# Kernel optimization log

Hardware: AMD Instinct MI355X
Metric: run time of the kernel (lower is better)

The kernel has to match this reference:

```python
import jax, jax.numpy as jnp
import numpy as np

B, C, H, W = 2, 128, 128, 128
K, STRIDE, DIL, NH = 8, 2, 2, 8
HID = int(C * 4 / 3)  # 170


def _ln(x, g, b):
    # layernorm2d: normalize over channel axis (last axis in NHWC)
    mu = jnp.mean(x, axis=-1, keepdims=True)
    xc = x - mu
    var = jnp.mean(xc * xc, axis=-1, keepdims=True)
    return xc * jax.lax.rsqrt(var + 1e-6) * g + b


def _nat_attn(xn, qkv_w, qkv_b, qg, qb, kg, kb, proj_w, proj_b):
    # dilated/strided local-neighborhood attention (NATTEN-style)
    Bq, Hq, Wq, Cq = xn.shape
    dh = Cq // NH
    qkv = xn @ qkv_w.T + qkv_b
    q, k, v = jnp.split(qkv, 3, axis=-1)
    q = _ln(q, qg, qb)
    k = _ln(k, kg, kb)
    # keys/values on a stride-subsampled grid
    kc = k[:, ::STRIDE, ::STRIDE, :]
    vc = v[:, ::STRIDE, ::STRIDE, :]
    Hc, Wc = Hq // STRIDE, Wq // STRIDE
    plo = DIL * (K // 2)
    phi = DIL * (K - 1 - K // 2)
    pad = ((0, 0), (plo, phi), (plo, phi), (0, 0))
    kp = jnp.pad(kc, pad)
    vp = jnp.pad(vc, pad)
    mp = jnp.pad(jnp.ones((1, Hc, Wc, 1), dtype=bool), pad)
    offs = [(i * DIL, j * DIL) for i in range(K) for j in range(K)]  # fixed k*k window taps
    kn = jnp.stack([kp[:, a:a + Hc, b:b + Wc, :] for a, b in offs], axis=3).reshape(Bq, Hc, Wc, K * K, NH, dh)
    vn = jnp.stack([vp[:, a:a + Hc, b:b + Wc, :] for a, b in offs], axis=3).reshape(Bq, Hc, Wc, K * K, NH, dh)
    mn = jnp.stack([mp[:, a:a + Hc, b:b + Wc, 0] for a, b in offs], axis=3)  # [1,Hc,Wc,kk]
    # each full-res query maps to its coarse kv cell: [B,Hc,stride,Wc,stride,heads,dh]
    q6 = q.reshape(Bq, Hc, STRIDE, Wc, STRIDE, NH, dh)
    scores = jnp.einsum('bisjtnd,bijknd->bisjtnk', q6, kn) * (dh ** -0.5)
    m = mn[:, :, None, :, None, None, :]
    scores = jnp.where(m, scores, jnp.float32(-1e30))
    attn = jax.nn.softmax(scores, axis=-1)
    out = jnp.einsum('bisjtnk,bijknd->bisjtnd', attn, vn).reshape(Bq, Hq, Wq, Cq)
    return out @ proj_w.T + proj_b


def _cffn(xn, fc1_w, fc1_b, mg, mb, fc2_w, fc2_b):
    h = xn @ fc1_w.T + fc1_b
    h = _ln(h, mg, mb)
    h = jax.nn.gelu(h, approximate=True)  # gelu_tanh
    return h @ fc2_w.T + fc2_b


def setup_inputs():
    key = jax.random.key(0)
    ks = jax.random.split(key, 6)
    w = lambda k, shp: jax.random.normal(k, shp, dtype=jnp.float32) * 0.02
    z = lambda n: jnp.zeros((n,), jnp.float32)
    o = lambda n: jnp.ones((n,), jnp.float32)
    return {
        'x': jax.random.normal(ks[0], (B, C, H, W), dtype=jnp.float32),
        'qkv_w': w(ks[1], (3 * C, C)), 'qkv_b': z(3 * C),
        'qg': o(C), 'qb': z(C), 'kg': o(C), 'kb': z(C),
        'proj_w': w(ks[2], (C, C)), 'proj_b': z(C),
        'n1g': o(C), 'n1b': z(C), 'n2g': o(C), 'n2b': z(C),
        'ls1_g': jnp.full((C,), 1e-5, jnp.float32),
        'ls2_g': jnp.full((C,), 1e-5, jnp.float32),
        'fc1_w': w(ks[3], (HID, C)), 'fc1_b': z(HID),
        'mg': o(HID), 'mb': z(HID),
        'fc2_w': w(ks[4], (C, HID)), 'fc2_b': z(C),
    }


def reference(x, qkv_w, qkv_b, qg, qb, kg, kb, proj_w, proj_b, n1g, n1b, n2g, n2b, ls1_g, ls2_g, fc1_w, fc1_b, mg, mb, fc2_w, fc2_b):
    xh = jnp.transpose(x, (0, 2, 3, 1))  # NCHW -> NHWC
    xh = xh + ls1_g * _nat_attn(_ln(xh, n1g, n1b), qkv_w, qkv_b, qg, qb, kg, kb, proj_w, proj_b)
    xh = xh + ls2_g * _cffn(_ln(xh, n2g, n2b), fc1_w, fc1_b, mg, mb, fc2_w, fc2_b)
    return jnp.transpose(xh, (0, 3, 1, 2))
```

## Files before the change

kernel.cpp:

```cpp
#include <hip/hip_runtime.h>
#include <hip/hip_bf16.h>

typedef __hip_bfloat16 BF;
typedef __attribute__((ext_vector_type(8))) short bf16x8;
typedef __attribute__((ext_vector_type(4))) float f32x4;
typedef __attribute__((ext_vector_type(4))) unsigned short us4;


#define ASTR 200
#define KSTR 136

__device__ __forceinline__ short bfr(float f){
  union{float f; unsigned u;} c; c.f = f;
  const unsigned u = c.u + 0x7FFFu + ((c.u >> 16) & 1u);
  return (short)(u >> 16);
}
__device__ __forceinline__ bf16x8 pk8(float4 a, float4 b){
  bf16x8 r;
  r[0]=bfr(a.x); r[1]=bfr(a.y); r[2]=bfr(a.z); r[3]=bfr(a.w);
  r[4]=bfr(b.x); r[5]=bfr(b.y); r[6]=bfr(b.z); r[7]=bfr(b.w);
  return r;
}

__device__ __forceinline__ void gsum16h(float v[16], float* red, int tid){
  #pragma unroll
  for(int s = 1; s < 64; s <<= 1){
    #pragma unroll
    for(int i = 0; i < 16; i++) v[i] += __shfl_xor(v[i], s);
  }
  const int wid = tid >> 6, half = tid >> 7;
  __syncthreads();
  if((tid & 63) == 0){
    #pragma unroll
    for(int i = 0; i < 16; i++) red[wid*16 + i] = v[i];
  }
  __syncthreads();
  #pragma unroll
  for(int i = 0; i < 16; i++) v[i] = red[half*32 + i] + red[half*32 + 16 + i];
}

__device__ __forceinline__ void rowredh(float s1[4], float s2[4], float* red, int tid){
  const int lane = tid & 63, wid = tid >> 6, half = tid >> 7;
  #pragma unroll
  for(int m = 1; m < 16; m <<= 1){
    #pragma unroll
    for(int r = 0; r < 4; r++){ s1[r] += __shfl_xor(s1[r], m); s2[r] += __shfl_xor(s2[r], m); }
  }
  const int q4 = lane >> 4;
  __syncthreads();
  if((lane & 15) == 0){
    #pragma unroll
    for(int r = 0; r < 4; r++){
      red[wid*32 + q4*4 + r]      = s1[r];
      red[wid*32 + 16 + q4*4 + r] = s2[r];
    }
  }
  __syncthreads();
  #pragma unroll
  for(int r = 0; r < 4; r++){
    s1[r] = red[half*64 + q4*4 + r]      + red[half*64 + 32 + q4*4 + r];
    s2[r] = red[half*64 + 16 + q4*4 + r] + red[half*64 + 48 + q4*4 + r];
  }
}

__device__ __forceinline__ void rowred4(float s1[4], float s2[4], float* red,
                                        int wave, int lane){
  #pragma unroll
  for(int m = 1; m < 16; m <<= 1){
    #pragma unroll
    for(int r = 0; r < 4; r++){ s1[r] += __shfl_xor(s1[r], m); s2[r] += __shfl_xor(s2[r], m); }
  }
  const int q4 = lane >> 4;
  __syncthreads();
  if((lane & 15) == 0){
    #pragma unroll
    for(int r = 0; r < 4; r++){
      red[wave*32 + q4*4 + r]      = s1[r];
      red[wave*32 + 16 + q4*4 + r] = s2[r];
    }
  }
  __syncthreads();
  #pragma unroll
  for(int r = 0; r < 4; r++){
    s1[r] = red[q4*4 + r] + red[32 + q4*4 + r] + red[64 + q4*4 + r] + red[96 + q4*4 + r];
    s2[r] = red[16 + q4*4 + r] + red[48 + q4*4 + r] + red[80 + q4*4 + r] + red[112 + q4*4 + r];
  }
}

__global__ void __launch_bounds__(256)
k_pre(const float* __restrict__ x,
      const float* __restrict__ qkv_w, const float* __restrict__ proj_w,
      const float* __restrict__ fc1_w, const float* __restrict__ fc2_w,
      const float* __restrict__ qkv_b,
      const float* __restrict__ kg, const float* __restrict__ kb,
      const float* __restrict__ n1g, const float* __restrict__ n1b,
      float* __restrict__ xt, BF* __restrict__ pk,
      float* __restrict__ kcb, float* __restrict__ vcb){
  __shared__ __align__(16) unsigned char sm[16640];
  const int bx = blockIdx.x, tid = threadIdx.x;

  if(bx >= 952){
    float (*tile)[65] = (float(*)[65])sm;
    const int bxt = bx - 952;
    const int b = bxt >> 9, r2 = bxt & 511;
    const int pb = (r2 & 255) * 64, cb = (r2 >> 8) * 64;
    const int tx = tid & 63, ty = tid >> 6;
    #pragma unroll
    for(int r = 0; r < 64; r += 4)
      tile[ty+r][tx] = x[(size_t)(b*128 + cb+ty+r)*16384 + pb + tx];
    __syncthreads();
    #pragma unroll
    for(int r = 0; r < 64; r += 4)
      xt[(size_t)((b<<14) + pb + ty + r)*128 + cb + tx] = tile[tx][ty+r];
    return;
  }
  if(bx >= 512){
    const int idx = (bx - 512) * 256 + tid;
    if(idx >= 112640) return;
    float val;
    if(idx < 49152){
      const int reg = idx >> 14, l = idx & 16383;
      const int j = l & 7, q = (l>>3)&3, n = (l>>5)&127, s = l>>12;
      val = qkv_w[(reg*128 + n)*128 + (s*32 + q*8 + j)];
    } else if(idx < 65536){
      const int l = idx - 49152;
      const int j = l&7, q=(l>>3)&3, n=(l>>5)&127, s=l>>12;
      val = proj_w[n*128 + (s*32+q*8+j)];
    } else if(idx < 88064){
      const int l = idx - 65536;
      const int j = l&7, q=(l>>3)&3, rem = l>>5;
      const int n = rem % 176, s = rem / 176;
      const int k = s*32+q*8+j;
      val = (n < 170) ? fc1_w[n*128 + k] : 0.f;
    } else {
      const int l = idx - 88064;
      const int j = l&7, q=(l>>3)&3, n=(l>>5)&127, s=l>>12;
      const int k = s*32+q*8+j;
      val = (k < 170) ? fc2_w[n*170 + k] : 0.f;
    }
    pk[idx] = __float2bfloat16(val);
    return;
  }

  BF* const Abuf = (BF*)sm;
  float* const red = (float*)(sm + 8704);
  const int lane = tid & 63, half = tid >> 7, wh = (tid >> 6) & 1, c = tid & 127;
  const int l15 = lane & 15, q4 = lane >> 4;
  const int cp0 = bx * 16;
  const int b = cp0 >> 12, ic = (cp0 & 4095) >> 6, jb = cp0 & 63;
  BF* const AbufH = Abuf + half*16*KSTR;

  float xv[8];
  {
    const size_t off = (size_t)(b*128 + c)*16384 + (size_t)(2*ic)*128 + 2*(jb + half*8);
    const float4* xp4 = (const float4*)(x + off);
    const float4 f0 = xp4[0], f1 = xp4[1], f2 = xp4[2], f3 = xp4[3];
    xv[0]=f0.x; xv[1]=f0.z; xv[2]=f1.x; xv[3]=f1.z;
    xv[4]=f2.x; xv[5]=f2.z; xv[6]=f3.x; xv[7]=f3.z;
  }
  float st[16];
  #pragma unroll
  for(int r = 0; r < 8; r++){ st[r] = xv[r]; st[8+r] = xv[r]*xv[r]; }
  gsum16h(st, red, tid);
  {
    const float g = n1g[c], be = n1b[c];
    #pragma unroll
    for(int r = 0; r < 8; r++){
      const float mu = st[r]*(1.f/128.f);
      const float var = st[8+r]*(1.f/128.f) - mu*mu;
      AbufH[r*KSTR + c] = __float2bfloat16((xv[r]-mu)*rsqrtf(var+1e-6f)*g + be);
    }
  }
  __syncthreads();
  bf16x8 af[4];
  #pragma unroll
  for(int s = 0; s < 4; s++) af[s] = *(const bf16x8*)&AbufH[l15*KSTR + s*32 + q4*8];

  f32x4 acc[4];
  #pragma unroll
  for(int nt = 0; nt < 4; nt++){ acc[nt][0]=0.f; acc[nt][1]=0.f; acc[nt][2]=0.f; acc[nt][3]=0.f; }
  #pragma unroll
  for(int nt = 0; nt < 4; nt++){
    const int n = (wh*4+nt)*16 + l15;
    #pragma unroll
    for(int s = 0; s < 4; s++){
      const float* wp = qkv_w + (size_t)(128 + n)*128 + s*32 + q4*8;
      acc[nt] = __builtin_amdgcn_mfma_f32_16x16x32_bf16(
        af[s], pk8(*(const float4*)wp, *(const float4*)(wp+4)), acc[nt], 0,0,0);
    }
  }
  float s1[4], s2[4];
  #pragma unroll
  for(int r = 0; r < 4; r++){ s1[r]=0.f; s2[r]=0.f; }
  #pragma unroll
  for(int nt = 0; nt < 4; nt++){
    const float colb = qkv_b[128 + (wh*4+nt)*16 + l15];
    #pragma unroll
    for(int r = 0; r < 4; r++){
      const float vv = acc[nt][r] + colb;
      acc[nt][r] = vv; s1[r] += vv; s2[r] += vv*vv;
    }
  }
  rowredh(s1, s2, red, tid);
  #pragma unroll
  for(int nt = 0; nt < 4; nt++){
    const int col = (wh*4+nt)*16 + l15;
    const float g = kg[col], be = kb[col];
    #pragma unroll
    for(int r = 0; r < 4; r++){
      const int row = q4*4 + r;
      if(row < 8){
        const float mu = s1[r]*(1.f/128.f);
        const float var = s2[r]*(1.f/128.f) - mu*mu;
        kcb[(size_t)(cp0 + half*8 + row)*128 + col] = (acc[nt][r]-mu)*rsqrtf(var+1e-6f)*g + be;
      }
    }
  }
  #pragma unroll
  for(int nt = 0; nt < 4; nt++){ acc[nt][0]=0.f; acc[nt][1]=0.f; acc[nt][2]=0.f; acc[nt][3]=0.f; }
  #pragma unroll
  for(int nt = 0; nt < 4; nt++){
    const int n = (wh*4+nt)*16 + l15;
    #pragma unroll
    for(int s = 0; s < 4; s++){
      const float* wp = qkv_w + (size_t)(256 + n)*128 + s*32 + q4*8;
      acc[nt] = __builtin_amdgcn_mfma_f32_16x16x32_bf16(
        af[s], pk8(*(const float4*)wp, *(const float4*)(wp+4)), acc[nt], 0,0,0);
    }
  }
  #pragma unroll
  for(int nt = 0; nt < 4; nt++){
    const int col = (wh*4+nt)*16 + l15;
    const float bv = qkv_b[256 + col];
    #pragma unroll
    for(int r = 0; r < 4; r++){
      const int row = q4*4 + r;
      if(row < 8) vcb[(size_t)(cp0 + half*8 + row)*128 + col] = acc[nt][r] + bv;
    }
  }
}

__global__ void __launch_bounds__(256, 5)
k_cell(const float* __restrict__ xt_in,
       const BF* __restrict__ packQ, const BF* __restrict__ packP,
       const BF* __restrict__ packF1, const BF* __restrict__ packF2,
       const float* __restrict__ qkv_b,
       const float* __restrict__ qg, const float* __restrict__ qb,
       const float* __restrict__ n1g, const float* __restrict__ n1b,
       const float* __restrict__ proj_b,
       const float* __restrict__ ls1, const float* __restrict__ ls2,
       const float* __restrict__ n2g, const float* __restrict__ n2b,
       const float* __restrict__ fc1_b,
       const float* __restrict__ mg, const float* __restrict__ mb,
       const float* __restrict__ fc2_b,
       const float* __restrict__ kcb, const float* __restrict__ vcb,
       float* __restrict__ out){
  __shared__ __align__(16) BF uni[9216];
  BF* const Abuf = uni;
  __shared__ float xvL[2048];
  __shared__ __align__(16) ushort qnH[2176];
  __shared__ ushort cidx2[256];
  float* const red = (float*)qnH;
  const int tid = threadIdx.x, wave = tid>>6, lane = tid&63;
  const int l15 = lane & 15, q4 = lane >> 4;

  const int bx0 = blockIdx.x;
  const int bx = ((bx0 & 7) << 8) | (bx0 >> 3);
  const int b = bx >> 10, rem = bx & 1023, ip = rem >> 5, jq = rem & 31;
  const size_t p0 = (size_t)b*2097152 + (size_t)(512*ip + 4*jq)*128;
  const int c = tid & 127, half = tid >> 7;

  float xv[8];
  #pragma unroll
  for(int r = 0; r < 8; r++){
    const int p = half*8 + r;
    const size_t pr = p0 + ((size_t)(p>>2)<<14) + (size_t)((p&3)<<7);
    xv[r] = xt_in[pr + c];
    xvL[p*128 + c] = xv[r];
  }
  {
    const int cell = tid >> 6, e = tid & 63;
    const int i = e >> 3, j = e & 7;
    const int ic = 2*ip + (cell>>1), jcc = 2*jq + (cell&1);
    const int ri = ic + 2*i - 8, rj = jcc + 2*j - 8;
    const bool ok = (rj >= 0) && (rj < 64) && (ri >= 0) && (ri < 64);
    cidx2[cell*64 + e] = ok ? (ushort)(b*4096 + ri*64 + rj) : (ushort)0;
  }

  float st[16];
  #pragma unroll
  for(int r = 0; r < 8; r++){ st[r] = xv[r]; st[8+r] = xv[r]*xv[r]; }
  gsum16h(st, red, tid);
  {
    const float g = n1g[c], be = n1b[c];
    #pragma unroll
    for(int r = 0; r < 8; r++){
      const int p = half*8 + r;
      const float mu = st[r]*(1.f/128.f);
      const float var = st[8+r]*(1.f/128.f) - mu*mu;
      Abuf[p*ASTR + c] = __float2bfloat16((xv[r]-mu)*rsqrtf(var+1e-6f)*g + be);
    }
  }
  __syncthreads();

  {
    bf16x8 af[4];
    #pragma unroll
    for(int s = 0; s < 4; s++) af[s] = *(const bf16x8*)&Abuf[l15*ASTR + s*32 + q4*8];
    f32x4 acc[2];
    #pragma unroll
    for(int nt = 0; nt < 2; nt++){ acc[nt][0]=0.f; acc[nt][1]=0.f; acc[nt][2]=0.f; acc[nt][3]=0.f; }
    #pragma unroll
    for(int nt = 0; nt < 2; nt++){
      const int n = (wave*2+nt)*16 + l15;
      #pragma unroll
      for(int s = 0; s < 4; s++){
        bf16x8 bf = *(const bf16x8*)&packQ[((s*128 + n)*4 + q4)*8];
        acc[nt] = __builtin_amdgcn_mfma_f32_16x16x32_bf16(af[s], bf, acc[nt], 0,0,0);
      }
    }
    float s1[4], s2[4];
    #pragma unroll
    for(int r = 0; r < 4; r++){ s1[r]=0.f; s2[r]=0.f; }
    #pragma unroll
    for(int nt = 0; nt < 2; nt++){
      const float cb2 = qkv_b[(wave*2+nt)*16 + l15];
      #pragma unroll
      for(int r = 0; r < 4; r++){
        const float vv = acc[nt][r] + cb2;
        acc[nt][r] = vv; s1[r] += vv; s2[r] += vv*vv;
      }
    }
    rowred4(s1, s2, red, wave, lane);
    short tw[2][4];
    {
      float mu[4], rs[4];
      #pragma unroll
      for(int r = 0; r < 4; r++){
        mu[r] = s1[r]*(1.f/128.f);
        rs[r] = rsqrtf(s2[r]*(1.f/128.f) - mu[r]*mu[r] + 1e-6f);
      }
      #pragma unroll
      for(int nt = 0; nt < 2; nt++){
        const int col = (wave*2+nt)*16 + l15;
        const float g = qg[col], be = qb[col];
        #pragma unroll
        for(int r = 0; r < 4; r++)
          tw[nt][r] = bfr((acc[nt][r]-mu[r])*rs[r]*g + be);
      }
    }
    __syncthreads();
    #pragma unroll
    for(int nt = 0; nt < 2; nt++){
      const int col = (wave*2+nt)*16 + l15;
      const int colp = col + (col >> 4);
      #pragma unroll
      for(int r = 0; r < 4; r++){
        const int cell = 2*(q4>>1) + ((r>>1)&1);
        const int lp   = 2*(q4&1) + (r&1);
        qnH[cell*544 + colp*4 + lp] = (ushort)tw[nt][r];
      }
    }
  }
  __syncthreads();

  const int hsub = l15 >> 2, px = l15 & 3;
  const int par = q4 >> 1, dbase = (q4 & 1) * 8;
  BF* const attw = uni + wave*2304;
  ushort* const Vt = (ushort*)attw;
  ushort* const Pb = (ushort*)(attw + 1152);
  const ushort* cidx = cidx2 + wave*64;
  const ushort* qp = qnH + wave*544;
  const int ic = 2*ip + (wave>>1), jcc = 2*jq + (wave&1);
  const int i0 = l15 >> 3;
  const int rj = jcc + 2*(l15 & 7) - 8;
  const bool vj = (rj >= 0) && (rj < 64);
  float madd[4];
  #pragma unroll
  for(int nt = 0; nt < 4; nt++){
    const int ri = ic + 2*(nt*2 + i0) - 8;
    madd[nt] = (vj && ri >= 0 && ri < 64) ? 0.f : -1e30f;
  }

  f32x4 oC[2];
  #pragma unroll
  for(int hg = 0; hg < 2; hg++){
    bf16x8 afq0, afq1;
    {
      const int idx0 = (hg*64 + hsub*16 + dbase + (hg*4 + hsub))*4 + px;
      short bq[8];
      #pragma unroll
      for(int j = 0; j < 8; j++) bq[j] = (short)qp[idx0 + 4*j];
      const bool a0 = (par == hsub), a1 = ((2 + par) == hsub);
      #pragma unroll
      for(int j = 0; j < 8; j++){
        afq0[j] = a0 ? bq[j] : (short)0;
        afq1[j] = a1 ? bq[j] : (short)0;
      }
    }
    f32x4 accq[4];
    #pragma unroll
    for(int nt = 0; nt < 4; nt++){ accq[nt][0]=0.f; accq[nt][1]=0.f; accq[nt][2]=0.f; accq[nt][3]=0.f; }
    #pragma unroll
    for(int nt = 0; nt < 4; nt++){
      const float* kp = kcb + ((size_t)cidx[nt*16 + l15] << 7) + hg*64 + q4*8;
      const float4 k00 = *(const float4*)kp;
      const float4 k01 = *(const float4*)(kp + 4);
      const float4 k10 = *(const float4*)(kp + 32);
      const float4 k11 = *(const float4*)(kp + 36);
      accq[nt] = __builtin_amdgcn_mfma_f32_16x16x32_bf16(afq0, pk8(k00,k01), accq[nt], 0,0,0);
      accq[nt] = __builtin_amdgcn_mfma_f32_16x16x32_bf16(afq1, pk8(k10,k11), accq[nt], 0,0,0);
    }
    float inv[4];
    #pragma unroll
    for(int reg = 0; reg < 4; reg++){
      const float s0 = accq[0][reg]*0.25f + madd[0];
      const float s1 = accq[1][reg]*0.25f + madd[1];
      const float s2 = accq[2][reg]*0.25f + madd[2];
      const float s3 = accq[3][reg]*0.25f + madd[3];
      float m = fmaxf(fmaxf(s0,s1), fmaxf(s2,s3));
      #pragma unroll
      for(int sft = 1; sft < 16; sft <<= 1) m = fmaxf(m, __shfl_xor(m, sft));
      const float e0 = __expf(s0-m), e1 = __expf(s1-m);
      const float e2 = __expf(s2-m), e3 = __expf(s3-m);
      ushort* pr = Pb + (q4*4 + reg)*72 + l15;
      pr[0]  = (ushort)bfr(e0);
      pr[16] = (ushort)bfr(e1);
      pr[32] = (ushort)bfr(e2);
      pr[48] = (ushort)bfr(e3);
      float es = e0+e1+e2+e3;
      #pragma unroll
      for(int sft = 1; sft < 16; sft <<= 1) es += __shfl_xor(es, sft);
      inv[reg] = 1.f/es;
    }
    const bf16x8 pa0 = *(const bf16x8*)(Pb + l15*72 + q4*8);
    const bf16x8 pa1 = *(const bf16x8*)(Pb + l15*72 + 32 + q4*8);

    f32x4 oSel; oSel[0]=0.f; oSel[1]=0.f; oSel[2]=0.f; oSel[3]=0.f;
    #pragma unroll
    for(int hs = 0; hs < 4; hs++){
      const int h = hg*4 + hs;
      float4 vv[4];
      #pragma unroll
      for(int it = 0; it < 4; it++)
        vv[it] = *(const float4*)(vcb + ((size_t)cidx[l15*4 + it] << 7) + h*16 + q4*4);
      #pragma unroll
      for(int dd = 0; dd < 4; dd++){
        us4 w;
        w[0] = (unsigned short)bfr(((const float*)&vv[0])[dd]);
        w[1] = (unsigned short)bfr(((const float*)&vv[1])[dd]);
        w[2] = (unsigned short)bfr(((const float*)&vv[2])[dd]);
        w[3] = (unsigned short)bfr(((const float*)&vv[3])[dd]);
        *(us4*)(Vt + (q4*4 + dd)*72 + l15*4) = w;
      }
      const bf16x8 bv0 = *(const bf16x8*)(Vt + l15*72 + q4*8);
      const bf16x8 bv1 = *(const bf16x8*)(Vt + l15*72 + 32 + q4*8);
      f32x4 accv; accv[0]=0.f; accv[1]=0.f; accv[2]=0.f; accv[3]=0.f;
      accv = __builtin_amdgcn_mfma_f32_16x16x32_bf16(pa0, bv0, accv, 0,0,0);
      accv = __builtin_amdgcn_mfma_f32_16x16x32_bf16(pa1, bv1, accv, 0,0,0);
      if(q4 == hs){ oSel[0]=accv[0]; oSel[1]=accv[1]; oSel[2]=accv[2]; oSel[3]=accv[3]; }
    }
    oC[hg][0] = oSel[0]*inv[0]; oC[hg][1] = oSel[1]*inv[1];
    oC[hg][2] = oSel[2]*inv[2]; oC[hg][3] = oSel[3]*inv[3];
  }
  __syncthreads();
  {
    ushort* ab = (ushort*)Abuf;
    #pragma unroll
    for(int hg = 0; hg < 2; hg++){
      const int col = (hg*4 + q4)*16 + l15;
      #pragma unroll
      for(int reg = 0; reg < 4; reg++){
        const int row_p = 8*(wave>>1) + 4*(reg>>1) + 2*(wave&1) + (reg&1);
        ab[row_p*ASTR + col] = (ushort)bfr(oC[hg][reg]);
      }
    }
  }
  __syncthreads();

  float xh[2][4];
  {
    bf16x8 af[4];
    #pragma unroll
    for(int s = 0; s < 4; s++) af[s] = *(const bf16x8*)&Abuf[l15*ASTR + s*32 + q4*8];
    f32x4 acc[2];
    #pragma unroll
    for(int nt = 0; nt < 2; nt++){ acc[nt][0]=0.f; acc[nt][1]=0.f; acc[nt][2]=0.f; acc[nt][3]=0.f; }
    #pragma unroll
    for(int nt = 0; nt < 2; nt++){
      const int n = (wave*2+nt)*16 + l15;
      #pragma unroll
      for(int s = 0; s < 4; s++){
        bf16x8 bf = *(const bf16x8*)&packP[((s*128 + n)*4 + q4)*8];
        acc[nt] = __builtin_amdgcn_mfma_f32_16x16x32_bf16(af[s], bf, acc[nt], 0,0,0);
      }
    }
    float s1[4], s2[4];
    #pragma unroll
    for(int r = 0; r < 4; r++){ s1[r]=0.f; s2[r]=0.f; }
    #pragma unroll
    for(int nt = 0; nt < 2; nt++){
      const int col = (wave*2+nt)*16 + l15;
      const float bp = proj_b[col], l1 = ls1[col];
      #pragma unroll
      for(int r = 0; r < 4; r++){
        const int p = q4*4 + r;
        const float hx = xvL[p*128 + col] + l1*(acc[nt][r] + bp);
        xh[nt][r] = hx; s1[r] += hx; s2[r] += hx*hx;
      }
    }
    rowred4(s1, s2, red, wave, lane);
    #pragma unroll
    for(int nt = 0; nt < 2; nt++){
      const int col = (wave*2+nt)*16 + l15;
      const float g2 = n2g[col], be = n2b[col];
      #pragma unroll
      for(int r = 0; r < 4; r++){
        const int p = q4*4 + r;
        const float mu = s1[r]*(1.f/128.f);
        const float var = s2[r]*(1.f/128.f) - mu*mu;
        Abuf[p*ASTR + col] =
          __float2bfloat16((xh[nt][r]-mu)*rsqrtf(var+1e-6f)*g2 + be);
      }
    }
  }
  __syncthreads();

  {
    bf16x8 af[4];
    #pragma unroll
    for(int s = 0; s < 4; s++) af[s] = *(const bf16x8*)&Abuf[l15*ASTR + s*32 + q4*8];
    const int NT1 = (wave < 3) ? 3 : 2;
    const int tb  = (wave < 3) ? wave*3 : 9;
    f32x4 acc1[3];
    #pragma unroll
    for(int nt = 0; nt < 3; nt++){ acc1[nt][0]=0.f; acc1[nt][1]=0.f; acc1[nt][2]=0.f; acc1[nt][3]=0.f; }
    for(int nt = 0; nt < NT1; nt++){
      const int n = (tb + nt)*16 + l15;
      #pragma unroll
      for(int s = 0; s < 4; s++){
        bf16x8 bf = *(const bf16x8*)&packF1[((s*176 + n)*4 + q4)*8];
        acc1[nt] = __builtin_amdgcn_mfma_f32_16x16x32_bf16(af[s], bf, acc1[nt], 0,0,0);
      }
    }
    float s1[4], s2[4];
    #pragma unroll
    for(int r = 0; r < 4; r++){ s1[r]=0.f; s2[r]=0.f; }
    for(int nt = 0; nt < NT1; nt++){
      const int col = (tb + nt)*16 + l15;
      const float b1 = (col < 170) ? fc1_b[col] : 0.f;
      #pragma unroll
      for(int r = 0; r < 4; r++){
        const float vv = acc1[nt][r] + b1;
        acc1[nt][r] = vv; s1[r] += vv; s2[r] += vv*vv;
      }
    }
    rowred4(s1, s2, red, wave, lane);
    for(int z = tid; z < 352; z += 256){
      const int row = z / 22, colz = 170 + (z - (z/22)*22);
      Abuf[row*ASTR + colz] = __float2bfloat16(0.f);
    }
    const float kA = 0.7978845608028654f, kB = 0.044715f;
    for(int nt = 0; nt < NT1; nt++){
      const int col = (tb + nt)*16 + l15;
      if(col < 170){
        const float g2 = mg[col], be = mb[col];
        #pragma unroll
        for(int r = 0; r < 4; r++){
          const int p = q4*4 + r;
          const float mu = s1[r]*(1.f/170.f);
          const float var = s2[r]*(1.f/170.f) - mu*mu;
          const float hn = (acc1[nt][r]-mu)*rsqrtf(var+1e-6f)*g2 + be;
          const float u = kA*(hn + kB*hn*hn*hn);
          const float gl = hn / (1.f + __expf(-2.f*u));
          Abuf[p*ASTR + col] = __float2bfloat16(gl);
        }
      }
    }
  }
  __syncthreads();

  {
    bf16x8 af[6];
    #pragma unroll
    for(int s = 0; s < 6; s++) af[s] = *(const bf16x8*)&Abuf[l15*ASTR + s*32 + q4*8];
    f32x4 acc[2];
    #pragma unroll
    for(int nt = 0; nt < 2; nt++){ acc[nt][0]=0.f; acc[nt][1]=0.f; acc[nt][2]=0.f; acc[nt][3]=0.f; }
    #pragma unroll
    for(int nt = 0; nt < 2; nt++){
      const int n = (wave*2+nt)*16 + l15;
      #pragma unroll
      for(int s = 0; s < 6; s++){
        bf16x8 bf = *(const bf16x8*)&packF2[((s*128 + n)*4 + q4)*8];
        acc[nt] = __builtin_amdgcn_mfma_f32_16x16x32_bf16(af[s], bf, acc[nt], 0,0,0);
      }
    }
    #pragma unroll
    for(int nt = 0; nt < 2; nt++){
      const int col = (wave*2+nt)*16 + l15;
      const float bf2 = fc2_b[col], l2 = ls2[col];
      float4 o4;
      o4.x = xh[nt][0] + l2*(acc[nt][0] + bf2);
      o4.y = xh[nt][1] + l2*(acc[nt][1] + bf2);
      o4.z = xh[nt][2] + l2*(acc[nt][2] + bf2);
      o4.w = xh[nt][3] + l2*(acc[nt][3] + bf2);
      *(float4*)(out + (size_t)(b*128 + col)*16384 + (size_t)(4*ip + q4)*128 + 4*jq) = o4;
    }
  }
}

extern "C" void kernel_launch(void* const* d_in, const int* in_sizes, int n_in,
                              void* d_out, int out_size, void* d_ws, size_t ws_size,
                              hipStream_t stream){
  const float* x      = (const float*)d_in[0];
  const float* qkv_w  = (const float*)d_in[1];
  const float* qkv_b  = (const float*)d_in[2];
  const float* qg     = (const float*)d_in[3];
  const float* qb     = (const float*)d_in[4];
  const float* kg     = (const float*)d_in[5];
  const float* kb     = (const float*)d_in[6];
  const float* proj_w = (const float*)d_in[7];
  const float* proj_b = (const float*)d_in[8];
  const float* n1g    = (const float*)d_in[9];
  const float* n1b    = (const float*)d_in[10];
  const float* n2g    = (const float*)d_in[11];
  const float* n2b    = (const float*)d_in[12];
  const float* ls1    = (const float*)d_in[13];
  const float* ls2    = (const float*)d_in[14];
  const float* fc1_w  = (const float*)d_in[15];
  const float* fc1_b  = (const float*)d_in[16];
  const float* mg     = (const float*)d_in[17];
  const float* mb     = (const float*)d_in[18];
  const float* fc2_w  = (const float*)d_in[19];
  const float* fc2_b  = (const float*)d_in[20];

  float* ws  = (float*)d_ws;
  float* xt  = ws;
  float* kcb = ws + 4194304;
  float* vcb = ws + 5242880;
  BF* pk     = (BF*)(ws + 6291456);
  BF* packQ  = pk;
  BF* packP  = pk + 49152;
  BF* packF1 = pk + 65536;
  BF* packF2 = pk + 88064;

  k_pre <<<1976, 256, 0, stream>>>(x, qkv_w, proj_w, fc1_w, fc2_w, qkv_b,
                                   kg, kb, n1g, n1b, xt, pk, kcb, vcb);
  k_cell<<<2048, 256, 0, stream>>>(xt, packQ, packP, packF1, packF2,
                                   qkv_b, qg, qb, n1g, n1b, proj_b, ls1, ls2,
                                   n2g, n2b, fc1_b, mg, mb, fc2_b,
                                   kcb, vcb, (float*)d_out);
}
```

Measured before the change: 234.4 us.

## Fuse pre and cell kernels into one persistent cooperative kernel with grid sync

Merges the preprocessing kernel (K/V projection, transpose, weight packing) and the per-cell attention/FFN kernel into a single cooperative launch of 1280 blocks. The blocks finish the pre-work, hit a grid-wide barrier, then loop over the 2048 cell units. The pre-work is redistributed so some blocks handle two transpose tiles, and a two-kernel path is kept in case the cooperative launch fails. This removes one kernel launch and its tail gap, at the cost of a grid barrier, the restrictions of cooperative launch, and possible load imbalance because units do not divide evenly across blocks.

```diff
diff --git a/kernel.cpp b/kernel.cpp
--- a/kernel.cpp
+++ b/kernel.cpp
@@ -1,5 +1,8 @@
 #include <hip/hip_runtime.h>
+#include <hip/hip_cooperative_groups.h>
 #include <hip/hip_bf16.h>
+
+namespace cg = cooperative_groups;
 
 typedef __hip_bfloat16 BF;
 typedef __attribute__((ext_vector_type(8))) short bf16x8;
@@ -9,6 +12,14 @@
 
 #define ASTR 200
 #define KSTR 136
+
+struct KP {
+  const float *x, *qkv_w, *proj_w, *fc1_w, *fc2_w, *qkv_b;
+  const float *qg, *qb, *kg, *kb, *n1g, *n1b, *proj_b, *ls1, *ls2;
+  const float *n2g, *n2b, *fc1_b, *mg, *mb, *fc2_b;
+  float *xt, *kcb, *vcb, *out;
+  BF *pk;
+};
 
 __device__ __forceinline__ short bfr(float f){
   union{float f; unsigned u;} c; c.f = f;
@@ -87,185 +98,168 @@
   }
 }
 
-__global__ void __launch_bounds__(256)
-k_pre(const float* __restrict__ x,
-      const float* __restrict__ qkv_w, const float* __restrict__ proj_w,
-      const float* __restrict__ fc1_w, const float* __restrict__ fc2_w,
-      const float* __restrict__ qkv_b,
-      const float* __restrict__ kg, const float* __restrict__ kb,
-      const float* __restrict__ n1g, const float* __restrict__ n1b,
-      float* __restrict__ xt, BF* __restrict__ pk,
-      float* __restrict__ kcb, float* __restrict__ vcb){
-  __shared__ __align__(16) unsigned char sm[16640];
-  const int bx = blockIdx.x, tid = threadIdx.x;
-
-  if(bx >= 952){
-    float (*tile)[65] = (float(*)[65])sm;
-    const int bxt = bx - 952;
-    const int b = bxt >> 9, r2 = bxt & 511;
+__device__ __forceinline__ void pre_work(const KP& P, BF* uni, float* red){
+  const int bid = blockIdx.x, tid = threadIdx.x;
+  if(bid < 512){
+    BF* const Abuf = uni;
+    const int lane = tid & 63, half = tid >> 7, wh = (tid >> 6) & 1, c = tid & 127;
+    const int l15 = lane & 15, q4 = lane >> 4;
+    const int cp0 = bid * 16;
+    const int b = cp0 >> 12, ic = (cp0 & 4095) >> 6, jb = cp0 & 63;
+    BF* const AbufH = Abuf + half*16*KSTR;
+
+    float xv[8];
+    {
+      const size_t off = (size_t)(b*128 + c)*16384 + (size_t)(2*ic)*128 + 2*(jb + half*8);
+      const float4* xp4 = (const float4*)(P.x + off);
+      const float4 f0 = xp4[0], f1 = xp4[1], f2 = xp4[2], f3 = xp4[3];
+      xv[0]=f0.x; xv[1]=f0.z; xv[2]=f1.x; xv[3]=f1.z;
+      xv[4]=f2.x; xv[5]=f2.z; xv[6]=f3.x; xv[7]=f3.z;
+    }
+    float st[16];
+    #pragma unroll
+    for(int r = 0; r < 8; r++){ st[r] = xv[r]; st[8+r] = xv[r]*xv[r]; }
+    gsum16h(st, red, tid);
+    {
+      const float g = P.n1g[c], be = P.n1b[c];
+      #pragma unroll
+      for(int r = 0; r < 8; r++){
+        const float mu = st[r]*(1.f/128.f);
+        const float var = st[8+r]*(1.f/128.f) - mu*mu;
+        AbufH[r*KSTR + c] = __float2bfloat16((xv[r]-mu)*rsqrtf(var+1e-6f)*g + be);
+      }
+    }
+    __syncthreads();
+    bf16x8 af[4];
+    #pragma unroll
+    for(int s = 0; s < 4; s++) af[s] = *(const bf16x8*)&AbufH[l15*KSTR + s*32 + q4*8];
+
+    f32x4 acc[4];
+    #pragma unroll
+    for(int nt = 0; nt < 4; nt++){ acc[nt][0]=0.f; acc[nt][1]=0.f; acc[nt][2]=0.f; acc[nt][3]=0.f; }
+    #pragma unroll
+    for(int nt = 0; nt < 4; nt++){
+      const int n = (wh*4+nt)*16 + l15;
+      #pragma unroll
+      for(int s = 0; s < 4; s++){
+        const float* wp = P.qkv_w + (size_t)(128 + n)*128 + s*32 + q4*8;
+        acc[nt] = __builtin_amdgcn_mfma_f32_16x16x32_bf16(
+          af[s], pk8(*(const float4*)wp, *(const float4*)(wp+4)), acc[nt], 0,0,0);
+      }
+    }
+    float s1[4], s2[4];
+    #pragma unroll
+    for(int r = 0; r < 4; r++){ s1[r]=0.f; s2[r]=0.f; }
+    #pragma unroll
+    for(int nt = 0; nt < 4; nt++){
+      const float colb = P.qkv_b[128 + (wh*4+nt)*16 + l15];
+      #pragma unroll
+      for(int r = 0; r < 4; r++){
+        const float vv = acc[nt][r] + colb;
+        acc[nt][r] = vv; s1[r] += vv; s2[r] += vv*vv;
+      }
+    }
+    rowredh(s1, s2, red, tid);
+    #pragma unroll
+    for(int nt = 0; nt < 4; nt++){
+      const int col = (wh*4+nt)*16 + l15;
+      const float g = P.kg[col], be = P.kb[col];
+      #pragma unroll
+      for(int r = 0; r < 4; r++){
+        const int row = q4*4 + r;
+        if(row < 8){
+          const float mu = s1[r]*(1.f/128.f);
+          const float var = s2[r]*(1.f/128.f) - mu*mu;
+          P.kcb[(size_t)(cp0 + half*8 + row)*128 + col] =
+            (acc[nt][r]-mu)*rsqrtf(var+1e-6f)*g + be;
+        }
+      }
+    }
+    #pragma unroll
+    for(int nt = 0; nt < 4; nt++){ acc[nt][0]=0.f; acc[nt][1]=0.f; acc[nt][2]=0.f; acc[nt][3]=0.f; }
+    #pragma unroll
+    for(int nt = 0; nt < 4; nt++){
+      const int n = (wh*4+nt)*16 + l15;
+      #pragma unroll
+      for(int s = 0; s < 4; s++){
+        const float* wp = P.qkv_w + (size_t)(256 + n)*128 + s*32 + q4*8;
+        acc[nt] = __builtin_amdgcn_mfma_f32_16x16x32_bf16(
+          af[s], pk8(*(const float4*)wp, *(const float4*)(wp+4)), acc[nt], 0,0,0);
+      }
+    }
+    #pragma unroll
+    for(int nt = 0; nt < 4; nt++){
+      const int col = (wh*4+nt)*16 + l15;
+      const float bv = P.qkv_b[256 + col];
+      #pragma unroll
+      for(int r = 0; r < 4; r++){
+        const int row = q4*4 + r;
+        if(row < 8) P.vcb[(size_t)(cp0 + half*8 + row)*128 + col] = acc[nt][r] + bv;
+      }
+    }
+    return;
+  }
+
+  float (*tile)[65] = (float(*)[65])uni;
+  const int t0 = bid - 512;
+  const int ntile = (bid < 768) ? 2 : 1;
+  for(int it = 0; it < ntile; it++){
+    const int t = t0 + it*768;
+    const int b = t >> 9, r2 = t & 511;
     const int pb = (r2 & 255) * 64, cb = (r2 >> 8) * 64;
     const int tx = tid & 63, ty = tid >> 6;
+    if(it) __syncthreads();
     #pragma unroll
     for(int r = 0; r < 64; r += 4)
-      tile[ty+r][tx] = x[(size_t)(b*128 + cb+ty+r)*16384 + pb + tx];
+      tile[ty+r][tx] = P.x[(size_t)(b*128 + cb+ty+r)*16384 + pb + tx];
     __syncthreads();
     #pragma unroll
     for(int r = 0; r < 64; r += 4)
-      xt[(size_t)((b<<14) + pb + ty + r)*128 + cb + tx] = tile[tx][ty+r];
-    return;
-  }
-  if(bx >= 512){
-    const int idx = (bx - 512) * 256 + tid;
-    if(idx >= 112640) return;
-    float val;
-    if(idx < 49152){
-      const int reg = idx >> 14, l = idx & 16383;
-      const int j = l & 7, q = (l>>3)&3, n = (l>>5)&127, s = l>>12;
-      val = qkv_w[(reg*128 + n)*128 + (s*32 + q*8 + j)];
-    } else if(idx < 65536){
-      const int l = idx - 49152;
-      const int j = l&7, q=(l>>3)&3, n=(l>>5)&127, s=l>>12;
-      val = proj_w[n*128 + (s*32+q*8+j)];
-    } else if(idx < 88064){
-      const int l = idx - 65536;
-      const int j = l&7, q=(l>>3)&3, rem = l>>5;
-      const int n = rem % 176, s = rem / 176;
-      const int k = s*32+q*8+j;
-      val = (n < 170) ? fc1_w[n*128 + k] : 0.f;
-    } else {
-      const int l = idx - 88064;
-      const int j = l&7, q=(l>>3)&3, n=(l>>5)&127, s=l>>12;
-      const int k = s*32+q*8+j;
-      val = (k < 170) ? fc2_w[n*170 + k] : 0.f;
-    }
-    pk[idx] = __float2bfloat16(val);
-    return;
-  }
-
-  BF* const Abuf = (BF*)sm;
-  float* const red = (float*)(sm + 8704);
-  const int lane = tid & 63, half = tid >> 7, wh = (tid >> 6) & 1, c = tid & 127;
-  const int l15 = lane & 15, q4 = lane >> 4;
-  const int cp0 = bx * 16;
-  const int b = cp0 >> 12, ic = (cp0 & 4095) >> 6, jb = cp0 & 63;
-  BF* const AbufH = Abuf + half*16*KSTR;
-
-  float xv[8];
-  {
-    const size_t off = (size_t)(b*128 + c)*16384 + (size_t)(2*ic)*128 + 2*(jb + half*8);
-    const float4* xp4 = (const float4*)(x + off);
-    const float4 f0 = xp4[0], f1 = xp4[1], f2 = xp4[2], f3 = xp4[3];
-    xv[0]=f0.x; xv[1]=f0.z; xv[2]=f1.x; xv[3]=f1.z;
-    xv[4]=f2.x; xv[5]=f2.z; xv[6]=f3.x; xv[7]=f3.z;
-  }
-  float st[16];
-  #pragma unroll
-  for(int r = 0; r < 8; r++){ st[r] = xv[r]; st[8+r] = xv[r]*xv[r]; }
-  gsum16h(st, red, tid);
-  {
-    const float g = n1g[c], be = n1b[c];
-    #pragma unroll
-    for(int r = 0; r < 8; r++){
-      const float mu = st[r]*(1.f/128.f);
-      const float var = st[8+r]*(1.f/128.f) - mu*mu;
-      AbufH[r*KSTR + c] = __float2bfloat16((xv[r]-mu)*rsqrtf(var+1e-6f)*g + be);
-    }
-  }
-  __syncthreads();
-  bf16x8 af[4];
-  #pragma unroll
-  for(int s = 0; s < 4; s++) af[s] = *(const bf16x8*)&AbufH[l15*KSTR + s*32 + q4*8];
-
-  f32x4 acc[4];
-  #pragma unroll
-  for(int nt = 0; nt < 4; nt++){ acc[nt][0]=0.f; acc[nt][1]=0.f; acc[nt][2]=0.f; acc[nt][3]=0.f; }
-  #pragma unroll
-  for(int nt = 0; nt < 4; nt++){
-    const int n = (wh*4+nt)*16 + l15;
-    #pragma unroll
-    for(int s = 0; s < 4; s++){
-      const float* wp = qkv_w + (size_t)(128 + n)*128 + s*32 + q4*8;
-      acc[nt] = __builtin_amdgcn_mfma_f32_16x16x32_bf16(
-        af[s], pk8(*(const float4*)wp, *(const float4*)(wp+4)), acc[nt], 0,0,0);
-    }
-  }
-  float s1[4], s2[4];
-  #pragma unroll
-  for(int r = 0; r < 4; r++){ s1[r]=0.f; s2[r]=0.f; }
-  #pragma unroll
-  for(int nt = 0; nt < 4; nt++){
-    const float colb = qkv_b[128 + (wh*4+nt)*16 + l15];
-    #pragma unroll
-    for(int r = 0; r < 4; r++){
-      const float vv = acc[nt][r] + colb;
-      acc[nt][r] = vv; s1[r] += vv; s2[r] += vv*vv;
-    }
-  }
-  rowredh(s1, s2, red, tid);
-  #pragma unroll
-  for(int nt = 0; nt < 4; nt++){
-    const int col = (wh*4+nt)*16 + l15;
-    const float g = kg[col], be = kb[col];
-    #pragma unroll
-    for(int r = 0; r < 4; r++){
-      const int row = q4*4 + r;
-      if(row < 8){
-        const float mu = s1[r]*(1.f/128.f);
-        const float var = s2[r]*(1.f/128.f) - mu*mu;
-        kcb[(size_t)(cp0 + half*8 + row)*128 + col] = (acc[nt][r]-mu)*rsqrtf(var+1e-6f)*g + be;
-      }
-    }
-  }
-  #pragma unroll
-  for(int nt = 0; nt < 4; nt++){ acc[nt][0]=0.f; acc[nt][1]=0.f; acc[nt][2]=0.f; acc[nt][3]=0.f; }
-  #pragma unroll
-  for(int nt = 0; nt < 4; nt++){
-    const int n = (wh*4+nt)*16 + l15;
-    #pragma unroll
-    for(int s = 0; s < 4; s++){
-      const float* wp = qkv_w + (size_t)(256 + n)*128 + s*32 + q4*8;
-      acc[nt] = __builtin_amdgcn_mfma_f32_16x16x32_bf16(
-        af[s], pk8(*(const float4*)wp, *(const float4*)(wp+4)), acc[nt], 0,0,0);
-    }
-  }
-  #pragma unroll
-  for(int nt = 0; nt < 4; nt++){
-    const int col = (wh*4+nt)*16 + l15;
-    const float bv = qkv_b[256 + col];
-    #pragma unroll
-    for(int r = 0; r < 4; r++){
-      const int row = q4*4 + r;
-      if(row < 8) vcb[(size_t)(cp0 + half*8 + row)*128 + col] = acc[nt][r] + bv;
-    }
-  }
-}
-
-__global__ void __launch_bounds__(256, 5)
-k_cell(const float* __restrict__ xt_in,
-       const BF* __restrict__ packQ, const BF* __restrict__ packP,
-       const BF* __restrict__ packF1, const BF* __restrict__ packF2,
-       const float* __restrict__ qkv_b,
-       const float* __restrict__ qg, const float* __restrict__ qb,
-       const float* __restrict__ n1g, const float* __restrict__ n1b,
-       const float* __restrict__ proj_b,
-       const float* __restrict__ ls1, const float* __restrict__ ls2,
-       const float* __restrict__ n2g, const float* __restrict__ n2b,
-       const float* __restrict__ fc1_b,
-       const float* __restrict__ mg, const float* __restrict__ mb,
-       const float* __restrict__ fc2_b,
-       const float* __restrict__ kcb, const float* __restrict__ vcb,
-       float* __restrict__ out){
-  __shared__ __align__(16) BF uni[9216];
-  BF* const Abuf = uni;
-  __shared__ float xvL[2048];
-  __shared__ __align__(16) ushort qnH[2176];
-  __shared__ ushort cidx2[256];
-  float* const red = (float*)qnH;
+      P.xt[(size_t)((b<<14) + pb + ty + r)*128 + cb + tx] = tile[tx][ty+r];
+  }
+  if(bid >= 768){
+    const int idx = (bid - 768) * 256 + tid;
+    if(idx < 112640){
+      float val;
+      if(idx < 49152){
+        const int reg = idx >> 14, l = idx & 16383;
+        const int j = l & 7, q = (l>>3)&3, n = (l>>5)&127, s = l>>12;
+        val = P.qkv_w[(reg*128 + n)*128 + (s*32 + q*8 + j)];
+      } else if(idx < 65536){
+        const int l = idx - 49152;
+        const int j = l&7, q=(l>>3)&3, n=(l>>5)&127, s=l>>12;
+        val = P.proj_w[n*128 + (s*32+q*8+j)];
+      } else if(idx < 88064){
+        const int l = idx - 65536;
+        const int j = l&7, q=(l>>3)&3, rem = l>>5;
+        const int n = rem % 176, s = rem / 176;
+        const int k = s*32+q*8+j;
+        val = (n < 170) ? P.fc1_w[n*128 + k] : 0.f;
+      } else {
+        const int l = idx - 88064;
+        const int j = l&7, q=(l>>3)&3, n=(l>>5)&127, s=l>>12;
+        const int k = s*32+q*8+j;
+        val = (k < 170) ? P.fc2_w[n*170 + k] : 0.f;
+      }
+      P.pk[idx] = __float2bfloat16(val);
+    }
+  }
+}
+
+__device__ __forceinline__ void cell_unit(const KP& P, int u,
+                                          BF* uni, float* xvL,
+                                          ushort* qnH, ushort* cidx2){
   const int tid = threadIdx.x, wave = tid>>6, lane = tid&63;
   const int l15 = lane & 15, q4 = lane >> 4;
-
-  const int bx0 = blockIdx.x;
-  const int bx = ((bx0 & 7) << 8) | (bx0 >> 3);
+  BF* const Abuf = uni;
+  float* const red = (float*)qnH;
+  const BF* packQ  = P.pk;
+  const BF* packP  = P.pk + 49152;
+  const BF* packF1 = P.pk + 65536;
+  const BF* packF2 = P.pk + 88064;
+  __syncthreads();
+
+  const int bx = ((u & 7) << 8) | (u >> 3);
   const int b = bx >> 10, rem = bx & 1023, ip = rem >> 5, jq = rem & 31;
   const size_t p0 = (size_t)b*2097152 + (size_t)(512*ip + 4*jq)*128;
   const int c = tid & 127, half = tid >> 7;
@@ -275,7 +269,7 @@
   for(int r = 0; r < 8; r++){
     const int p = half*8 + r;
     const size_t pr = p0 + ((size_t)(p>>2)<<14) + (size_t)((p&3)<<7);
-    xv[r] = xt_in[pr + c];
+    xv[r] = P.xt[pr + c];
     xvL[p*128 + c] = xv[r];
   }
   {
@@ -292,7 +286,7 @@
   for(int r = 0; r < 8; r++){ st[r] = xv[r]; st[8+r] = xv[r]*xv[r]; }
   gsum16h(st, red, tid);
   {
-    const float g = n1g[c], be = n1b[c];
+    const float g = P.n1g[c], be = P.n1b[c];
     #pragma unroll
     for(int r = 0; r < 8; r++){
       const int p = half*8 + r;
@@ -324,7 +318,7 @@
     for(int r = 0; r < 4; r++){ s1[r]=0.f; s2[r]=0.f; }
     #pragma unroll
     for(int nt = 0; nt < 2; nt++){
-      const float cb2 = qkv_b[(wave*2+nt)*16 + l15];
+      const float cb2 = P.qkv_b[(wave*2+nt)*16 + l15];
       #pragma unroll
       for(int r = 0; r < 4; r++){
         const float vv = acc[nt][r] + cb2;
@@ -343,7 +337,7 @@
       #pragma unroll
       for(int nt = 0; nt < 2; nt++){
         const int col = (wave*2+nt)*16 + l15;
-        const float g = qg[col], be = qb[col];
+        const float g = P.qg[col], be = P.qb[col];
         #pragma unroll
         for(int r = 0; r < 4; r++)
           tw[nt][r] = bfr((acc[nt][r]-mu[r])*rs[r]*g + be);
@@ -403,7 +397,7 @@
     for(int nt = 0; nt < 4; nt++){ accq[nt][0]=0.f; accq[nt][1]=0.f; accq[nt][2]=0.f; accq[nt][3]=0.f; }
     #pragma unroll
     for(int nt = 0; nt < 4; nt++){
-      const float* kp = kcb + ((size_t)cidx[nt*16 + l15] << 7) + hg*64 + q4*8;
+      const float* kp = P.kcb + ((size_t)cidx[nt*16 + l15] << 7) + hg*64 + q4*8;
       const float4 k00 = *(const float4*)kp;
       const float4 k01 = *(const float4*)(kp + 4);
       const float4 k10 = *(const float4*)(kp + 32);
@@ -443,7 +437,7 @@
       float4 vv[4];
       #pragma unroll
       for(int it = 0; it < 4; it++)
-        vv[it] = *(const float4*)(vcb + ((size_t)cidx[l15*4 + it] << 7) + h*16 + q4*4);
+        vv[it] = *(const float4*)(P.vcb + ((size_t)cidx[l15*4 + it] << 7) + h*16 + q4*4);
       #pragma unroll
       for(int dd = 0; dd < 4; dd++){
         us4 w;
@@ -501,7 +495,7 @@
     #pragma unroll
     for(int nt = 0; nt < 2; nt++){
       const int col = (wave*2+nt)*16 + l15;
-      const float bp = proj_b[col], l1 = ls1[col];
+      const float bp = P.proj_b[col], l1 = P.ls1[col];
       #pragma unroll
       for(int r = 0; r < 4; r++){
         const int p = q4*4 + r;
@@ -513,7 +507,7 @@
     #pragma unroll
     for(int nt = 0; nt < 2; nt++){
       const int col = (wave*2+nt)*16 + l15;
-      const float g2 = n2g[col], be = n2b[col];
+      const float g2 = P.n2g[col], be = P.n2b[col];
       #pragma unroll
       for(int r = 0; r < 4; r++){
         const int p = q4*4 + r;
@@ -548,7 +542,7 @@
     for(int r = 0; r < 4; r++){ s1[r]=0.f; s2[r]=0.f; }
     for(int nt = 0; nt < NT1; nt++){
       const int col = (tb + nt)*16 + l15;
-      const float b1 = (col < 170) ? fc1_b[col] : 0.f;
+      const float b1 = (col < 170) ? P.fc1_b[col] : 0.f;
       #pragma unroll
       for(int r = 0; r < 4; r++){
         const float vv = acc1[nt][r] + b1;
@@ -564,15 +558,15 @@
     for(int nt = 0; nt < NT1; nt++){
       const int col = (tb + nt)*16 + l15;
       if(col < 170){
-        const float g2 = mg[col], be = mb[col];
+        const float g2 = P.mg[col], be = P.mb[col];
         #pragma unroll
         for(int r = 0; r < 4; r++){
           const int p = q4*4 + r;
           const float mu = s1[r]*(1.f/170.f);
           const float var = s2[r]*(1.f/170.f) - mu*mu;
           const float hn = (acc1[nt][r]-mu)*rsqrtf(var+1e-6f)*g2 + be;
-          const float u = kA*(hn + kB*hn*hn*hn);
-          const float gl = hn / (1.f + __expf(-2.f*u));
+          const float u2 = kA*(hn + kB*hn*hn*hn);
+          const float gl = hn / (1.f + __expf(-2.f*u2));
           Abuf[p*ASTR + col] = __float2bfloat16(gl);
         }
       }
@@ -599,56 +593,91 @@
     #pragma unroll
     for(int nt = 0; nt < 2; nt++){
       const int col = (wave*2+nt)*16 + l15;
-      const float bf2 = fc2_b[col], l2 = ls2[col];
+      const float bf2 = P.fc2_b[col], l2 = P.ls2[col];
       float4 o4;
       o4.x = xh[nt][0] + l2*(acc[nt][0] + bf2);
       o4.y = xh[nt][1] + l2*(acc[nt][1] + bf2);
       o4.z = xh[nt][2] + l2*(acc[nt][2] + bf2);
       o4.w = xh[nt][3] + l2*(acc[nt][3] + bf2);
-      *(float4*)(out + (size_t)(b*128 + col)*16384 + (size_t)(4*ip + q4)*128 + 4*jq) = o4;
-    }
-  }
+      *(float4*)(P.out + (size_t)(b*128 + col)*16384 + (size_t)(4*ip + q4)*128 + 4*jq) = o4;
+    }
+  }
+}
+
+__global__ void __launch_bounds__(256, 5)
+k_fused(KP P){
+  __shared__ __align__(16) BF uni[9216];
+  __shared__ float xvL[2048];
+  __shared__ __align__(16) ushort qnH[2176];
+  __shared__ ushort cidx2[256];
+
+  pre_work(P, uni, (float*)qnH);
+  __threadfence();
+  cg::this_grid().sync();
+
+  const int bid = blockIdx.x;
+  #pragma unroll 1
+  for(int r = 0; r < 2; ++r){
+    const int u = bid + r*1280;
+    if(u < 2048) cell_unit(P, u, uni, xvL, qnH, cidx2);
+  }
+}
+
+__global__ void __launch_bounds__(256)
+k_preFB(KP P){
+  __shared__ __align__(16) BF uni[9216];
+  __shared__ __align__(16) ushort qnH[2176];
+  pre_work(P, uni, (float*)qnH);
+}
+
+__global__ void __launch_bounds__(256, 5)
+k_cellFB(KP P){
+  __shared__ __align__(16) BF uni[9216];
+  __shared__ float xvL[2048];
+  __shared__ __align__(16) ushort qnH[2176];
+  __shared__ ushort cidx2[256];
+  cell_unit(P, blockIdx.x, uni, xvL, qnH, cidx2);
 }
 
 extern "C" void kernel_launch(void* const* d_in, const int* in_sizes, int n_in,
                               void* d_out, int out_size, void* d_ws, size_t ws_size,
                               hipStream_t stream){
-  const float* x      = (const float*)d_in[0];
-  const float* qkv_w  = (const float*)d_in[1];
-  const float* qkv_b  = (const float*)d_in[2];
-  const float* qg     = (const float*)d_in[3];
-  const float* qb     = (const float*)d_in[4];
-  const float* kg     = (const float*)d_in[5];
-  const float* kb     = (const float*)d_in[6];
-  const float* proj_w = (const float*)d_in[7];
-  const float* proj_b = (const float*)d_in[8];
-  const float* n1g    = (const float*)d_in[9];
-  const float* n1b    = (const float*)d_in[10];
-  const float* n2g    = (const float*)d_in[11];
-  const float* n2b    = (const float*)d_in[12];
-  const float* ls1    = (const float*)d_in[13];
-  const float* ls2    = (const float*)d_in[14];
-  const float* fc1_w  = (const float*)d_in[15];
-  const float* fc1_b  = (const float*)d_in[16];
-  const float* mg     = (const float*)d_in[17];
-  const float* mb     = (const float*)d_in[18];
-  const float* fc2_w  = (const float*)d_in[19];
-  const float* fc2_b  = (const float*)d_in[20];
-
-  float* ws  = (float*)d_ws;
-  float* xt  = ws;
-  float* kcb = ws + 4194304;
-  float* vcb = ws + 5242880;
-  BF* pk     = (BF*)(ws + 6291456);
-  BF* packQ  = pk;
-  BF* packP  = pk + 49152;
-  BF* packF1 = pk + 65536;
-  BF* packF2 = pk + 88064;
-
-  k_pre <<<1976, 256, 0, stream>>>(x, qkv_w, proj_w, fc1_w, fc2_w, qkv_b,
-                                   kg, kb, n1g, n1b, xt, pk, kcb, vcb);
-  k_cell<<<2048, 256, 0, stream>>>(xt, packQ, packP, packF1, packF2,
-                                   qkv_b, qg, qb, n1g, n1b, proj_b, ls1, ls2,
-                                   n2g, n2b, fc1_b, mg, mb, fc2_b,
-                                   kcb, vcb, (float*)d_out);
-}
+  float* ws = (float*)d_ws;
+  KP p;
+  p.x      = (const float*)d_in[0];
+  p.qkv_w  = (const float*)d_in[1];
+  p.qkv_b  = (const float*)d_in[2];
+  p.qg     = (const float*)d_in[3];
+  p.qb     = (const float*)d_in[4];
+  p.kg     = (const float*)d_in[5];
+  p.kb     = (const float*)d_in[6];
+  p.proj_w = (const float*)d_in[7];
+  p.proj_b = (const float*)d_in[8];
+  p.n1g    = (const float*)d_in[9];
+  p.n1b    = (const float*)d_in[10];
+  p.n2g    = (const float*)d_in[11];
+  p.n2b    = (const float*)d_in[12];
+  p.ls1    = (const float*)d_in[13];
+  p.ls2    = (const float*)d_in[14];
+  p.fc1_w  = (const float*)d_in[15];
+  p.fc1_b  = (const float*)d_in[16];
+  p.mg     = (const float*)d_in[17];
+  p.mb     = (const float*)d_in[18];
+  p.fc2_w  = (const float*)d_in[19];
+  p.fc2_b  = (const float*)d_in[20];
+  p.xt  = ws;
+  p.kcb = ws + 4194304;
+  p.vcb = ws + 5242880;
+  p.pk  = (BF*)(ws + 6291456);
+  p.out = (float*)d_out;
+
+  void* args[] = {(void*)&p};
+  hipError_t err = hipLaunchCooperativeKernel(
+      reinterpret_cast<const void*>(&k_fused),
+      dim3(1280), dim3(256), args, 0, stream);
+  if(err != hipSuccess){
+    (void)hipGetLastError();
+    k_preFB <<<1280, 256, 0, stream>>>(p);
+    k_cellFB<<<2048, 256, 0, stream>>>(p);
+  }
+}
```

Result: slower. 580.4 us (+147.6%).
